# Kernel tuning notes

Hardware: AMD Instinct MI355X
Metric: run time of the kernel (lower is better)

Reference implementation:

```python
import jax, jax.numpy as jnp
import numpy as np

V = 50257; CTX = 2048; D = 1024; H = 16; L = 8; DH = D // H
B = 2; S = 2048; EPS = 1e-5


def setup_inputs() -> dict:
    key = jax.random.key(0)
    ks = jax.random.split(key, 8)
    s = 0.02
    def n(k, shape):
        return jax.random.normal(k, shape, jnp.float32) * s
    return {
        "x": jax.random.randint(ks[0], (B, S), 0, V),
        "wte": n(ks[1], (V, D)),
        "wpe": n(ks[2], (CTX, D)),
        "ln1_g": jnp.ones((L, D), jnp.float32), "ln1_b": jnp.zeros((L, D), jnp.float32),
        "w_qkv": n(ks[3], (L, D, 3 * D)), "b_qkv": jnp.zeros((L, 3 * D), jnp.float32),
        "w_proj": n(ks[4], (L, D, D)), "b_proj": jnp.zeros((L, D), jnp.float32),
        "ln2_g": jnp.ones((L, D), jnp.float32), "ln2_b": jnp.zeros((L, D), jnp.float32),
        "w_fc": n(ks[5], (L, D, 4 * D)), "b_fc": jnp.zeros((L, 4 * D), jnp.float32),
        "w_cp": n(ks[6], (L, 4 * D, D)), "b_cp": jnp.zeros((L, D), jnp.float32),
        "lnf_g": jnp.ones((D,), jnp.float32), "lnf_b": jnp.zeros((D,), jnp.float32),
        "w_head": n(ks[7], (D, V)),
    }


def layernorm(x, g, b):
    m = x.mean(-1, keepdims=True)
    v = ((x - m) ** 2).mean(-1, keepdims=True)
    return (x - m) * jax.lax.rsqrt(v + EPS) * g + b


def gpt_forward(x, wte, wpe, ln1_g, ln1_b, w_qkv, b_qkv, w_proj, b_proj,
                ln2_g, ln2_b, w_fc, b_fc, w_cp, b_cp, lnf_g, lnf_b, w_head):
    Bx, Sx = x.shape
    h = wte[x] + wpe[:Sx]                       # [B,S,D]
    mask = jnp.tril(jnp.ones((Sx, Sx), bool))   # causal mask
    scale = DH ** -0.5

    def block(h, p):
        g1, b1, wq, bq, wp, bp, g2, b2, wf, bf, wc, bc = p
        y = layernorm(h, g1, b1)
        qkv = y @ wq + bq                        # [B,S,3D]
        q, k, v = jnp.split(qkv, 3, axis=-1)
        q = q.reshape(Bx, Sx, H, DH)
        k = k.reshape(Bx, Sx, H, DH)
        v = v.reshape(Bx, Sx, H, DH)
        att = jnp.einsum('bqhd,bkhd->bhqk', q, k) * scale
        att = jnp.where(mask, att, -jnp.inf)
        att = jax.nn.softmax(att, axis=-1)
        z = jnp.einsum('bhqk,bkhd->bqhd', att, v).reshape(Bx, Sx, D)
        h = h + z @ wp + bp
        y2 = layernorm(h, g2, b2)
        h = h + jax.nn.gelu(y2 @ wf + bf, approximate=False) @ wc + bc
        return h, None

    h, _ = jax.lax.scan(block, h, (ln1_g, ln1_b, w_qkv, b_qkv, w_proj, b_proj,
                                   ln2_g, ln2_b, w_fc, b_fc, w_cp, b_cp))
    h = layernorm(h, lnf_g, lnf_b)
    logits = h[:, -1:, :] @ w_head              # [B,1,V] (last position only)
    return logits


def reference(x, wte, wpe, ln1_g, ln1_b, w_qkv, b_qkv, w_proj, b_proj,
              ln2_g, ln2_b, w_fc, b_fc, w_cp, b_cp, lnf_g, lnf_b, w_head):
    return gpt_forward(x, wte, wpe, ln1_g, ln1_b, w_qkv, b_qkv, w_proj, b_proj,
                       ln2_g, ln2_b, w_fc, b_fc, w_cp, b_cp, lnf_g, lnf_b, w_head)
```

## Files before the change

kernel.cpp:

```cpp
#include <hip/hip_runtime.h>
#include <hip/hip_bf16.h>
#include <math.h>

#define VOCAB 50257
#define CTX 2048
#define DMODEL 1024
#define NHEAD 16
#define NLAYER 8
#define DHEAD 64
#define BATCH 2
#define SEQ 2048
#define NTOK (BATCH * SEQ)

typedef __bf16 bf16x8 __attribute__((ext_vector_type(8)));
typedef float  f32x4  __attribute__((ext_vector_type(4)));
typedef unsigned short ushort4v __attribute__((ext_vector_type(4)));
typedef unsigned short ushort8v __attribute__((ext_vector_type(8)));

__device__ inline void gl_lds16(const void* g, void* l) {
    __builtin_amdgcn_global_load_lds(
        (const __attribute__((address_space(1))) unsigned int*)g,
        (__attribute__((address_space(3))) unsigned int*)l, 16, 0, 0);
}

__device__ inline unsigned short f2bs(float v) {
    __hip_bfloat16 t = __float2bfloat16(v);
    return *(unsigned short*)&t;
}

__global__ void embed_kernel(const int* __restrict__ x,
                             const float* __restrict__ wte,
                             const float* __restrict__ wpe,
                             float* __restrict__ h) {
    int t = blockIdx.x;
    int s = t & (SEQ - 1);
    int tok = x[t];
    const float* pe = wpe + (long)s * DMODEL;
    const float* te = wte + (long)tok * DMODEL;
    float* ph = h + (long)t * DMODEL;
    for (int d = threadIdx.x; d < DMODEL; d += 256)
        ph[d] = te[d] + pe[d];
}

__device__ inline float wave_sum(float v) {
    for (int off = 32; off; off >>= 1) v += __shfl_xor(v, off);
    return v;
}
__device__ inline void st_val(float* p, float v) { *p = v; }
__device__ inline void st_val(__hip_bfloat16* p, float v) { *p = __float2bfloat16(v); }

template<typename OT>
__global__ void ln_kernel(const float* __restrict__ in, OT* __restrict__ out,
                          const float* __restrict__ g, const float* __restrict__ b,
                          long row_stride) {
    int row = blockIdx.x;
    const float* px = in + (long)row * row_stride;
    OT* po = out + (long)row * DMODEL;
    int tid = threadIdx.x;
    int wid = tid >> 6, lane = tid & 63;

    float x[4];
    float s = 0.f;
    #pragma unroll
    for (int i = 0; i < 4; ++i) { x[i] = px[tid + i * 256]; s += x[i]; }
    s = wave_sum(s);
    __shared__ float red[4], red2[4];
    if (lane == 0) red[wid] = s;
    __syncthreads();
    float mean = (red[0] + red[1] + red[2] + red[3]) * (1.0f / DMODEL);

    float s2 = 0.f;
    #pragma unroll
    for (int i = 0; i < 4; ++i) { float d = x[i] - mean; s2 += d * d; }
    s2 = wave_sum(s2);
    if (lane == 0) red2[wid] = s2;
    __syncthreads();
    float var = (red2[0] + red2[1] + red2[2] + red2[3]) * (1.0f / DMODEL);
    float r = 1.0f / sqrtf(var + 1e-5f);
    #pragma unroll
    for (int i = 0; i < 4; ++i) {
        int d = tid + i * 256;
        st_val(po + d, (x[i] - mean) * r * g[d] + b[d]);
    }
}

__global__ void convT64(const float* __restrict__ W,
                        unsigned short* __restrict__ WT, int K, int N) {
    __shared__ float t[64][65];
    const int k0 = blockIdx.x * 64, n0 = blockIdx.y * 64;
    const int tid = threadIdx.x;
    {
        const int krow = tid >> 4, c4 = (tid & 15) * 4;
        #pragma unroll
        for (int p = 0; p < 4; ++p) {
            f32x4 gv = *(const f32x4*)&W[(long)(k0 + p * 16 + krow) * N + n0 + c4];
            #pragma unroll
            for (int j = 0; j < 4; ++j) t[p * 16 + krow][c4 + j] = gv[j];
        }
    }
    __syncthreads();
    {
        const int n = tid >> 3, kl = (tid & 7) * 8;
        #pragma unroll
        for (int p = 0; p < 2; ++p) {
            ushort8v pk;
            #pragma unroll
            for (int j = 0; j < 8; ++j) pk[j] = f2bs(t[kl + j][p * 32 + n]);
            *(ushort8v*)&WT[(long)(n0 + p * 32 + n) * K + k0 + kl] = pk;
        }
    }
}

template<int EPI>
__global__ __launch_bounds__(256)
void mm_mfma(const unsigned short* __restrict__ A,
             const unsigned short* __restrict__ BT,
             const float* __restrict__ bias, const float* __restrict__ R,
             void* __restrict__ Cout, int M, int N, int K) {
    __shared__ unsigned short As[128 * 32];
    __shared__ unsigned short Bs[128 * 32];
    const int tid = threadIdx.x;
    const int w = tid >> 6, lane = tid & 63;
    const int bm = blockIdx.y * 128, bn = blockIdx.x * 128;
    const int wr = (w >> 1) * 64, wc = (w & 1) * 64;

    f32x4 acc[4][4];
    #pragma unroll
    for (int m = 0; m < 4; ++m)
        #pragma unroll
        for (int n = 0; n < 4; ++n)
            acc[m][n] = (f32x4){0.f, 0.f, 0.f, 0.f};

    const int lrow = lane >> 2;
    const int lcol = (lane & 3) * 8;
    const unsigned short* gA = A + (long)(bm + w * 32 + lrow) * K + lcol;
    const unsigned short* gB = BT + (long)(bn + w * 32 + lrow) * K + lcol;
    unsigned short* lA = &As[(w * 32) * 32];
    unsigned short* lB = &Bs[(w * 32) * 32];

    for (int k0 = 0; k0 < K; k0 += 32) {
        gl_lds16(gA + k0,          lA);
        gl_lds16(gA + k0 + 16 * K, lA + 16 * 32);
        gl_lds16(gB + k0,          lB);
        gl_lds16(gB + k0 + 16 * K, lB + 16 * 32);
        __syncthreads();

        bf16x8 a[4], b[4];
        #pragma unroll
        for (int m = 0; m < 4; ++m)
            a[m] = *(const bf16x8*)&As[(wr + m * 16 + (lane & 15)) * 32 + (lane >> 4) * 8];
        #pragma unroll
        for (int n = 0; n < 4; ++n)
            b[n] = *(const bf16x8*)&Bs[(wc + n * 16 + (lane & 15)) * 32 + (lane >> 4) * 8];
        #pragma unroll
        for (int m = 0; m < 4; ++m)
            #pragma unroll
            for (int n = 0; n < 4; ++n)
                acc[m][n] = __builtin_amdgcn_mfma_f32_16x16x32_bf16(a[m], b[n], acc[m][n], 0, 0, 0);
        __syncthreads();
    }

    const int r0 = (lane >> 4) * 4, cc = lane & 15;
    #pragma unroll
    for (int n = 0; n < 4; ++n) {
        int colb = bn + wc + n * 16;
        float bv = bias[colb + cc];
        #pragma unroll
        for (int m = 0; m < 4; ++m) {
            int rowb = bm + wr + m * 16 + r0;
            if (EPI == 3) {
                unsigned short* qkvB = (unsigned short*)Cout;
                int which = colb >> 10, hh = (colb & 1023) >> 6, dbase = colb & 63;
                int b_ = rowb >> 11, s_ = rowb & 2047;
                long bh2 = b_ * 16 + hh;
                float v[4];
                #pragma unroll
                for (int r = 0; r < 4; ++r) v[r] = acc[m][n][r] + bv;
                if (which == 2) {
                    ushort4v pk;
                    #pragma unroll
                    for (int r = 0; r < 4; ++r) pk[r] = f2bs(v[r]);
                    *(ushort4v*)&qkvB[8388608L + (bh2 * 64 + dbase + cc) * 2048 + s_] = pk;
                } else {
                    unsigned short* dst = qkvB + (long)which * 4194304L +
                                          (bh2 * 2048 + s_) * 64 + dbase + cc;
                    #pragma unroll
                    for (int r = 0; r < 4; ++r) dst[r * 64] = f2bs(v[r]);
                }
            } else {
                #pragma unroll
                for (int r = 0; r < 4; ++r) {
                    long row = rowb + r, col = colb + cc;
                    float v = acc[m][n][r] + bv;
                    v = 0.5f * v * (1.0f + erff(v * 0.70710678118f));
                    ((__hip_bfloat16*)Cout)[row * N + col] = __float2bfloat16(v);
                }
            }
        }
    }
}

__global__ __launch_bounds__(256)
void mm_mfma_n64(const unsigned short* __restrict__ A,
                 const unsigned short* __restrict__ BT,
                 const float* __restrict__ bias, const float* __restrict__ R,
                 float* __restrict__ Cout, int M, int N, int K) {
    __shared__ unsigned short As[128 * 32];
    __shared__ unsigned short Bs[64 * 32];
    const int tid = threadIdx.x;
    const int w = tid >> 6, lane = tid & 63;
    const int bm = blockIdx.y * 128, bn = blockIdx.x * 64;
    const int wr = (w >> 1) * 64, wc = (w & 1) * 32;

    f32x4 acc[4][2];
    #pragma unroll
    for (int m = 0; m < 4; ++m)
        #pragma unroll
        for (int n = 0; n < 2; ++n)
            acc[m][n] = (f32x4){0.f, 0.f, 0.f, 0.f};

    const int lrow = lane >> 2;
    const int lcol = (lane & 3) * 8;
    const unsigned short* gA = A + (long)(bm + w * 32 + lrow) * K + lcol;
    const unsigned short* gB = BT + (long)(bn + w * 16 + lrow) * K + lcol;
    unsigned short* lA = &As[(w * 32) * 32];
    unsigned short* lB = &Bs[(w * 16) * 32];

    for (int k0 = 0; k0 < K; k0 += 32) {
        gl_lds16(gA + k0,          lA);
        gl_lds16(gA + k0 + 16 * K, lA + 16 * 32);
        gl_lds16(gB + k0,          lB);
        __syncthreads();

        bf16x8 a[4], b[2];
        #pragma unroll
        for (int m = 0; m < 4; ++m)
            a[m] = *(const bf16x8*)&As[(wr + m * 16 + (lane & 15)) * 32 + (lane >> 4) * 8];
        #pragma unroll
        for (int n = 0; n < 2; ++n)
            b[n] = *(const bf16x8*)&Bs[(wc + n * 16 + (lane & 15)) * 32 + (lane >> 4) * 8];
        #pragma unroll
        for (int m = 0; m < 4; ++m)
            #pragma unroll
            for (int n = 0; n < 2; ++n)
                acc[m][n] = __builtin_amdgcn_mfma_f32_16x16x32_bf16(a[m], b[n], acc[m][n], 0, 0, 0);
        __syncthreads();
    }

    const int r0 = (lane >> 4) * 4, cc = lane & 15;
    #pragma unroll
    for (int n = 0; n < 2; ++n) {
        int colb = bn + wc + n * 16;
        float bv = bias[colb + cc];
        #pragma unroll
        for (int m = 0; m < 4; ++m) {
            int rowb = bm + wr + m * 16 + r0;
            #pragma unroll
            for (int r = 0; r < 4; ++r) {
                long row = rowb + r, col = colb + cc;
                float v = acc[m][n][r] + bv + R[row * N + col];
                Cout[row * N + col] = v;
            }
        }
    }
}

__global__ __launch_bounds__(256)
void attn_mfma(const unsigned short* __restrict__ qB,
               const unsigned short* __restrict__ kB,
               const unsigned short* __restrict__ vT,
               __hip_bfloat16* __restrict__ z) {
    const int bh = blockIdx.x;
    const int qb = blockIdx.y * 64;
    const int tid = threadIdx.x, w = tid >> 6, lane = tid & 63;
    const int arow = lane & 15, kg = lane >> 4;
    __shared__ unsigned short Ks[128 * 64];
    __shared__ unsigned short Vs[64 * 128];
    __shared__ unsigned short Ps[4][16 * 128];

    const long kvbase = (long)bh * (2048 * 64);

    bf16x8 qa[2];
    {
        const unsigned short* q0 = qB + kvbase + (long)(qb + w * 16 + arow) * 64 + kg * 8;
        qa[0] = *(const bf16x8*)(q0);
        qa[1] = *(const bf16x8*)(q0 + 32);
    }

    f32x4 po[4];
    float mrow[4], lrow[4];
    #pragma unroll
    for (int i = 0; i < 4; ++i) {
        po[i] = (f32x4){0.f, 0.f, 0.f, 0.f};
        mrow[i] = -1e30f; lrow[i] = 0.f;
    }

    const int ksrow = lane >> 3;
    const int kschunk = (lane & 7) ^ ksrow;
    const int vsr = lane >> 4;
    const int cmax = qb >> 7;

    for (int c = 0; c <= cmax; ++c) {
        {
            const unsigned short* ks0 = kB + kvbase +
                (long)(c * 128 + w * 32 + ksrow) * 64 + kschunk * 8;
            #pragma unroll
            for (int i = 0; i < 4; ++i)
                gl_lds16(ks0 + (long)i * 8 * 64, &Ks[(w * 32 + i * 8) * 64]);
            #pragma unroll
            for (int i = 0; i < 4; ++i) {
                int d = w * 16 + i * 4 + vsr;
                int sch = (lane & 15) ^ (d & 7);
                gl_lds16(vT + kvbase + (long)d * 2048 + c * 128 + sch * 8,
                         &Vs[(w * 16 + i * 4) * 128]);
            }
        }
        __syncthreads();

        f32x4 s[8];
        #pragma unroll
        for (int n = 0; n < 8; ++n) {
            s[n] = (f32x4){0.f, 0.f, 0.f, 0.f};
            int row = n * 16 + arow, sw = row & 7;
            bf16x8 kb0 = *(const bf16x8*)&Ks[row * 64 + (kg ^ sw) * 8];
            bf16x8 kb1 = *(const bf16x8*)&Ks[row * 64 + ((4 + kg) ^ sw) * 8];
            s[n] = __builtin_amdgcn_mfma_f32_16x16x32_bf16(qa[0], kb0, s[n], 0, 0, 0);
            s[n] = __builtin_amdgcn_mfma_f32_16x16x32_bf16(qa[1], kb1, s[n], 0, 0, 0);
        }

        const bool diag = (c == cmax);
        #pragma unroll
        for (int n = 0; n < 8; ++n)
            #pragma unroll
            for (int r = 0; r < 4; ++r) {
                float v = s[n][r] * 0.125f;
                if (diag) {
                    int key = c * 128 + n * 16 + arow;
                    int qrow = qb + w * 16 + kg * 4 + r;
                    if (key > qrow) v = -1e30f;
                }
                s[n][r] = v;
            }

        #pragma unroll
        for (int r = 0; r < 4; ++r) {
            float rm = s[0][r];
            #pragma unroll
            for (int n = 1; n < 8; ++n) rm = fmaxf(rm, s[n][r]);
            #pragma unroll
            for (int off = 1; off < 16; off <<= 1)
                rm = fmaxf(rm, __shfl_xor(rm, off));
            float mnew = fmaxf(mrow[r], rm);
            float esc = expf(mrow[r] - mnew);
            float rs = 0.f;
            #pragma unroll
            for (int n = 0; n < 8; ++n) {
                float p = expf(s[n][r] - mnew);
                s[n][r] = p;
                rs += p;
            }
            #pragma unroll
            for (int off = 1; off < 16; off <<= 1)
                rs += __shfl_xor(rs, off);
            lrow[r] = lrow[r] * esc + rs;
            #pragma unroll
            for (int dt = 0; dt < 4; ++dt) po[dt][r] *= esc;
            mrow[r] = mnew;
        }

        #pragma unroll
        for (int n = 0; n < 8; ++n) {
            int col = n * 16 + arow;
            int chunk = col >> 3, cw = col & 7;
            #pragma unroll
            for (int r = 0; r < 4; ++r) {
                int row = kg * 4 + r;
                Ps[w][row * 128 + ((chunk ^ (row & 7)) * 8 + cw)] = f2bs(s[n][r]);
            }
        }

        bf16x8 pa[4];
        #pragma unroll
        for (int ks = 0; ks < 4; ++ks)
            pa[ks] = *(const bf16x8*)&Ps[w][arow * 128 + (((ks * 4 + kg) ^ (arow & 7)) * 8)];
        #pragma unroll
        for (int dt = 0; dt < 4; ++dt) {
            int vrow = dt * 16 + arow, sw = vrow & 7;
            #pragma unroll
            for (int ks = 0; ks < 4; ++ks) {
                bf16x8 vb = *(const bf16x8*)&Vs[vrow * 128 + (((ks * 4 + kg) ^ sw) * 8)];
                po[dt] = __builtin_amdgcn_mfma_f32_16x16x32_bf16(pa[ks], vb, po[dt], 0, 0, 0);
            }
        }
        __syncthreads();
    }

    const int b_ = bh >> 4, hofs = (bh & 15) * 64;
    #pragma unroll
    for (int dt = 0; dt < 4; ++dt)
        #pragma unroll
        for (int r = 0; r < 4; ++r) {
            long row = (long)b_ * 2048 + qb + w * 16 + kg * 4 + r;
            z[row * 1024 + hofs + dt * 16 + arow] = __float2bfloat16(po[dt][r] / lrow[r]);
        }
}

__global__ void head_kernel(const float* __restrict__ hl, const float* __restrict__ W,
                            float* __restrict__ out) {
    __shared__ float hs[2 * DMODEL];
    int tid = threadIdx.x;
    #pragma unroll
    for (int i = 0; i < 8; ++i) hs[tid + i * 256] = hl[tid + i * 256];
    __syncthreads();
    int v = blockIdx.x * 256 + tid;
    if (v >= VOCAB) return;
    float a0 = 0.f, a1 = 0.f;
    for (int d = 0; d < DMODEL; ++d) {
        float wv = W[(long)d * VOCAB + v];
        a0 += hs[d] * wv;
        a1 += hs[DMODEL + d] * wv;
    }
    out[v] = a0;
    out[VOCAB + v] = a1;
}

extern "C" void kernel_launch(void* const* d_in, const int* in_sizes, int n_in,
                              void* d_out, int out_size, void* d_ws, size_t ws_size,
                              hipStream_t stream) {
    const int*   x      = (const int*)  d_in[0];
    const float* wte    = (const float*)d_in[1];
    const float* wpe    = (const float*)d_in[2];
    const float* ln1_g  = (const float*)d_in[3];
    const float* ln1_b  = (const float*)d_in[4];
    const float* w_qkv  = (const float*)d_in[5];
    const float* b_qkv  = (const float*)d_in[6];
    const float* w_proj = (const float*)d_in[7];
    const float* b_proj = (const float*)d_in[8];
    const float* ln2_g  = (const float*)d_in[9];
    const float* ln2_b  = (const float*)d_in[10];
    const float* w_fc   = (const float*)d_in[11];
    const float* b_fc   = (const float*)d_in[12];
    const float* w_cp   = (const float*)d_in[13];
    const float* b_cp   = (const float*)d_in[14];
    const float* lnf_g  = (const float*)d_in[15];
    const float* lnf_b  = (const float*)d_in[16];
    const float* w_head = (const float*)d_in[17];
    float* out = (float*)d_out;

    char* ws = (char*)d_ws;
    float*          h     = (float*)ws;
    unsigned short* qkvB  = (unsigned short*)(ws + (16L << 20));
    __hip_bfloat16* y_bf  = (__hip_bfloat16*)(ws + (40L << 20));
    __hip_bfloat16* z_bf  = (__hip_bfloat16*)(ws + (48L << 20));
    __hip_bfloat16* fc_bf = (__hip_bfloat16*)(ws + (56L << 20));
    unsigned short* wT    = (unsigned short*)(ws + (88L << 20));
    float*          hl    = (float*)(ws + (97L << 20));

    embed_kernel<<<NTOK, 256, 0, stream>>>(x, wte, wpe, h);

    for (int l = 0; l < NLAYER; ++l) {
        ln_kernel<__hip_bfloat16><<<NTOK, 256, 0, stream>>>(
            h, y_bf, ln1_g + l * DMODEL, ln1_b + l * DMODEL, DMODEL);

        convT64<<<dim3(1024 / 64, 3072 / 64), 256, 0, stream>>>(
            w_qkv + (long)l * DMODEL * 3072, wT, 1024, 3072);
        mm_mfma<3><<<dim3(24, 32), 256, 0, stream>>>(
            (const unsigned short*)y_bf, wT, b_qkv + l * 3072, nullptr, qkvB,
            NTOK, 3072, 1024);

        attn_mfma<<<dim3(BATCH * NHEAD, SEQ / 64), 256, 0, stream>>>(
            qkvB, qkvB + 4194304L, qkvB + 8388608L, z_bf);

        convT64<<<dim3(1024 / 64, 1024 / 64), 256, 0, stream>>>(
            w_proj + (long)l * DMODEL * DMODEL, wT, 1024, 1024);
        mm_mfma_n64<<<dim3(16, 32), 256, 0, stream>>>(
            (const unsigned short*)z_bf, wT, b_proj + l * DMODEL, h, h,
            NTOK, 1024, 1024);

        ln_kernel<__hip_bfloat16><<<NTOK, 256, 0, stream>>>(
            h, y_bf, ln2_g + l * DMODEL, ln2_b + l * DMODEL, DMODEL);

        convT64<<<dim3(1024 / 64, 4096 / 64), 256, 0, stream>>>(
            w_fc + (long)l * DMODEL * 4096, wT, 1024, 4096);
        mm_mfma<2><<<dim3(32, 32), 256, 0, stream>>>(
            (const unsigned short*)y_bf, wT, b_fc + l * 4096, nullptr, fc_bf,
            NTOK, 4096, 1024);

        convT64<<<dim3(4096 / 64, 1024 / 64), 256, 0, stream>>>(
            w_cp + (long)l * 4096 * DMODEL, wT, 4096, 1024);
        mm_mfma_n64<<<dim3(16, 32), 256, 0, stream>>>(
            (const unsigned short*)fc_bf, wT, b_cp + l * DMODEL, h, h,
            NTOK, 1024, 4096);
    }

    ln_kernel<float><<<BATCH, 256, 0, stream>>>(h + (long)(SEQ - 1) * DMODEL, hl,
                                                lnf_g, lnf_b, (long)SEQ * DMODEL);
    head_kernel<<<(VOCAB + 255) / 256, 256, 0, stream>>>(hl, w_head, out);
}
```

Baseline: 2.727 ms.

## Co-schedule weight transpose kernels with LN, attention and FC via block-range fusion

Each weight conversion/transposition is folded into a neighbouring independent kernel (layernorm, attention, FC GEMM) through a block-index split, with two alternating wT buffers so the next weight can be prepared while the current one is consumed. This cuts kernel launches and lets the small, memory-bound transpose work overlap compute-bound work instead of running serially. Using dynamic shared memory sized for the larger branch can lower occupancy for the lighter branch, and mixed-block kernels may cause load imbalance.

```diff
diff --git a/kernel.cpp b/kernel.cpp
--- a/kernel.cpp
+++ b/kernel.cpp
@@ -46,16 +46,14 @@
     for (int off = 32; off; off >>= 1) v += __shfl_xor(v, off);
     return v;
 }
-__device__ inline void st_val(float* p, float v) { *p = v; }
-__device__ inline void st_val(__hip_bfloat16* p, float v) { *p = __float2bfloat16(v); }
-
-template<typename OT>
-__global__ void ln_kernel(const float* __restrict__ in, OT* __restrict__ out,
-                          const float* __restrict__ g, const float* __restrict__ b,
-                          long row_stride) {
-    int row = blockIdx.x;
-    const float* px = in + (long)row * row_stride;
-    OT* po = out + (long)row * DMODEL;
+
+__device__ void ln_body(char* smem, int row, const float* __restrict__ in,
+                        unsigned short* __restrict__ out,
+                        const float* __restrict__ g, const float* __restrict__ b) {
+    float* red  = (float*)smem;
+    float* red2 = red + 4;
+    const float* px = in + (long)row * DMODEL;
+    unsigned short* po = out + (long)row * DMODEL;
     int tid = threadIdx.x;
     int wid = tid >> 6, lane = tid & 63;
 
@@ -64,7 +62,6 @@
     #pragma unroll
     for (int i = 0; i < 4; ++i) { x[i] = px[tid + i * 256]; s += x[i]; }
     s = wave_sum(s);
-    __shared__ float red[4], red2[4];
     if (lane == 0) red[wid] = s;
     __syncthreads();
     float mean = (red[0] + red[1] + red[2] + red[3]) * (1.0f / DMODEL);
@@ -80,14 +77,46 @@
     #pragma unroll
     for (int i = 0; i < 4; ++i) {
         int d = tid + i * 256;
-        st_val(po + d, (x[i] - mean) * r * g[d] + b[d]);
-    }
-}
-
-__global__ void convT64(const float* __restrict__ W,
-                        unsigned short* __restrict__ WT, int K, int N) {
-    __shared__ float t[64][65];
-    const int k0 = blockIdx.x * 64, n0 = blockIdx.y * 64;
+        po[d] = f2bs((x[i] - mean) * r * g[d] + b[d]);
+    }
+}
+
+__global__ void ln_final(const float* __restrict__ in, float* __restrict__ out,
+                         const float* __restrict__ g, const float* __restrict__ b,
+                         long row_stride) {
+    __shared__ float red[4], red2[4];
+    int row = blockIdx.x;
+    const float* px = in + (long)row * row_stride;
+    float* po = out + (long)row * DMODEL;
+    int tid = threadIdx.x;
+    int wid = tid >> 6, lane = tid & 63;
+    float x[4];
+    float s = 0.f;
+    #pragma unroll
+    for (int i = 0; i < 4; ++i) { x[i] = px[tid + i * 256]; s += x[i]; }
+    s = wave_sum(s);
+    if (lane == 0) red[wid] = s;
+    __syncthreads();
+    float mean = (red[0] + red[1] + red[2] + red[3]) * (1.0f / DMODEL);
+    float s2 = 0.f;
+    #pragma unroll
+    for (int i = 0; i < 4; ++i) { float d = x[i] - mean; s2 += d * d; }
+    s2 = wave_sum(s2);
+    if (lane == 0) red2[wid] = s2;
+    __syncthreads();
+    float var = (red2[0] + red2[1] + red2[2] + red2[3]) * (1.0f / DMODEL);
+    float r = 1.0f / sqrtf(var + 1e-5f);
+    #pragma unroll
+    for (int i = 0; i < 4; ++i) {
+        int d = tid + i * 256;
+        po[d] = (x[i] - mean) * r * g[d] + b[d];
+    }
+}
+
+__device__ void convT_body(char* smem, int kx, int ny, const float* __restrict__ W,
+                           unsigned short* __restrict__ WT, int K, int N) {
+    float (*t)[65] = (float(*)[65])smem;
+    const int k0 = kx * 64, n0 = ny * 64;
     const int tid = threadIdx.x;
     {
         const int krow = tid >> 4, c4 = (tid & 15) * 4;
@@ -111,12 +140,11 @@
     }
 }
 
-template<int EPI>
 __global__ __launch_bounds__(256)
-void mm_mfma(const unsigned short* __restrict__ A,
-             const unsigned short* __restrict__ BT,
-             const float* __restrict__ bias, const float* __restrict__ R,
-             void* __restrict__ Cout, int M, int N, int K) {
+void mm_qkv(const unsigned short* __restrict__ A,
+            const unsigned short* __restrict__ BT,
+            const float* __restrict__ bias,
+            unsigned short* __restrict__ qkvB, int M, int N, int K) {
     __shared__ unsigned short As[128 * 32];
     __shared__ unsigned short Bs[128 * 32];
     const int tid = threadIdx.x;
@@ -168,33 +196,89 @@
         #pragma unroll
         for (int m = 0; m < 4; ++m) {
             int rowb = bm + wr + m * 16 + r0;
-            if (EPI == 3) {
-                unsigned short* qkvB = (unsigned short*)Cout;
-                int which = colb >> 10, hh = (colb & 1023) >> 6, dbase = colb & 63;
-                int b_ = rowb >> 11, s_ = rowb & 2047;
-                long bh2 = b_ * 16 + hh;
-                float v[4];
+            int which = colb >> 10, hh = (colb & 1023) >> 6, dbase = colb & 63;
+            int b_ = rowb >> 11, s_ = rowb & 2047;
+            long bh2 = b_ * 16 + hh;
+            float v[4];
+            #pragma unroll
+            for (int r = 0; r < 4; ++r) v[r] = acc[m][n][r] + bv;
+            if (which == 2) {
+                ushort4v pk;
                 #pragma unroll
-                for (int r = 0; r < 4; ++r) v[r] = acc[m][n][r] + bv;
-                if (which == 2) {
-                    ushort4v pk;
-                    #pragma unroll
-                    for (int r = 0; r < 4; ++r) pk[r] = f2bs(v[r]);
-                    *(ushort4v*)&qkvB[8388608L + (bh2 * 64 + dbase + cc) * 2048 + s_] = pk;
-                } else {
-                    unsigned short* dst = qkvB + (long)which * 4194304L +
-                                          (bh2 * 2048 + s_) * 64 + dbase + cc;
-                    #pragma unroll
-                    for (int r = 0; r < 4; ++r) dst[r * 64] = f2bs(v[r]);
-                }
+                for (int r = 0; r < 4; ++r) pk[r] = f2bs(v[r]);
+                *(ushort4v*)&qkvB[8388608L + (bh2 * 64 + dbase + cc) * 2048 + s_] = pk;
             } else {
+                unsigned short* dst = qkvB + (long)which * 4194304L +
+                                      (bh2 * 2048 + s_) * 64 + dbase + cc;
                 #pragma unroll
-                for (int r = 0; r < 4; ++r) {
-                    long row = rowb + r, col = colb + cc;
-                    float v = acc[m][n][r] + bv;
-                    v = 0.5f * v * (1.0f + erff(v * 0.70710678118f));
-                    ((__hip_bfloat16*)Cout)[row * N + col] = __float2bfloat16(v);
-                }
+                for (int r = 0; r < 4; ++r) dst[r * 64] = f2bs(v[r]);
+            }
+        }
+    }
+}
+
+__device__ void mm128_gelu_body(char* smem, int bx, int by,
+                                const unsigned short* __restrict__ A,
+                                const unsigned short* __restrict__ BT,
+                                const float* __restrict__ bias,
+                                unsigned short* __restrict__ Cout, int M, int N, int K) {
+    unsigned short* As = (unsigned short*)smem;
+    unsigned short* Bs = As + 128 * 32;
+    const int tid = threadIdx.x;
+    const int w = tid >> 6, lane = tid & 63;
+    const int bm = by * 128, bn = bx * 128;
+    const int wr = (w >> 1) * 64, wc = (w & 1) * 64;
+
+    f32x4 acc[4][4];
+    #pragma unroll
+    for (int m = 0; m < 4; ++m)
+        #pragma unroll
+        for (int n = 0; n < 4; ++n)
+            acc[m][n] = (f32x4){0.f, 0.f, 0.f, 0.f};
+
+    const int lrow = lane >> 2;
+    const int lcol = (lane & 3) * 8;
+    const unsigned short* gA = A + (long)(bm + w * 32 + lrow) * K + lcol;
+    const unsigned short* gB = BT + (long)(bn + w * 32 + lrow) * K + lcol;
+    unsigned short* lA = &As[(w * 32) * 32];
+    unsigned short* lB = &Bs[(w * 32) * 32];
+
+    for (int k0 = 0; k0 < K; k0 += 32) {
+        gl_lds16(gA + k0,          lA);
+        gl_lds16(gA + k0 + 16 * K, lA + 16 * 32);
+        gl_lds16(gB + k0,          lB);
+        gl_lds16(gB + k0 + 16 * K, lB + 16 * 32);
+        __syncthreads();
+
+        bf16x8 a[4], b[4];
+        #pragma unroll
+        for (int m = 0; m < 4; ++m)
+            a[m] = *(const bf16x8*)&As[(wr + m * 16 + (lane & 15)) * 32 + (lane >> 4) * 8];
+        #pragma unroll
+        for (int n = 0; n < 4; ++n)
+            b[n] = *(const bf16x8*)&Bs[(wc + n * 16 + (lane & 15)) * 32 + (lane >> 4) * 8];
+        #pragma unroll
+        for (int m = 0; m < 4; ++m)
+            #pragma unroll
+            for (int n = 0; n < 4; ++n)
+                acc[m][n] = __builtin_amdgcn_mfma_f32_16x16x32_bf16(a[m], b[n], acc[m][n], 0, 0, 0);
+        __syncthreads();
+    }
+
+    const int r0 = (lane >> 4) * 4, cc = lane & 15;
+    #pragma unroll
+    for (int n = 0; n < 4; ++n) {
+        int colb = bn + wc + n * 16;
+        float bv = bias[colb + cc];
+        #pragma unroll
+        for (int m = 0; m < 4; ++m) {
+            int rowb = bm + wr + m * 16 + r0;
+            #pragma unroll
+            for (int r = 0; r < 4; ++r) {
+                long row = rowb + r, col = colb + cc;
+                float v = acc[m][n][r] + bv;
+                v = 0.5f * v * (1.0f + erff(v * 0.70710678118f));
+                Cout[row * N + col] = f2bs(v);
             }
         }
     }
@@ -265,18 +349,16 @@
     }
 }
 
-__global__ __launch_bounds__(256)
-void attn_mfma(const unsigned short* __restrict__ qB,
-               const unsigned short* __restrict__ kB,
-               const unsigned short* __restrict__ vT,
-               __hip_bfloat16* __restrict__ z) {
-    const int bh = blockIdx.x;
-    const int qb = blockIdx.y * 64;
+__device__ void attn_body(char* smem, int bh, int qb,
+                          const unsigned short* __restrict__ qB,
+                          const unsigned short* __restrict__ kB,
+                          const unsigned short* __restrict__ vT,
+                          __hip_bfloat16* __restrict__ z) {
     const int tid = threadIdx.x, w = tid >> 6, lane = tid & 63;
     const int arow = lane & 15, kg = lane >> 4;
-    __shared__ unsigned short Ks[128 * 64];
-    __shared__ unsigned short Vs[64 * 128];
-    __shared__ unsigned short Ps[4][16 * 128];
+    unsigned short* Ks = (unsigned short*)smem;
+    unsigned short* Vs = Ks + 128 * 64;
+    unsigned short* Ps = Vs + 64 * 128 + w * 16 * 128;
 
     const long kvbase = (long)bh * (2048 * 64);
 
@@ -375,14 +457,14 @@
             #pragma unroll
             for (int r = 0; r < 4; ++r) {
                 int row = kg * 4 + r;
-                Ps[w][row * 128 + ((chunk ^ (row & 7)) * 8 + cw)] = f2bs(s[n][r]);
+                Ps[row * 128 + ((chunk ^ (row & 7)) * 8 + cw)] = f2bs(s[n][r]);
             }
         }
 
         bf16x8 pa[4];
         #pragma unroll
         for (int ks = 0; ks < 4; ++ks)
-            pa[ks] = *(const bf16x8*)&Ps[w][arow * 128 + (((ks * 4 + kg) ^ (arow & 7)) * 8)];
+            pa[ks] = *(const bf16x8*)&Ps[arow * 128 + (((ks * 4 + kg) ^ (arow & 7)) * 8)];
         #pragma unroll
         for (int dt = 0; dt < 4; ++dt) {
             int vrow = dt * 16 + arow, sw = vrow & 7;
@@ -403,6 +485,55 @@
             long row = (long)b_ * 2048 + qb + w * 16 + kg * 4 + r;
             z[row * 1024 + hofs + dt * 16 + arow] = __float2bfloat16(po[dt][r] / lrow[r]);
         }
+}
+
+__global__ __launch_bounds__(256)
+void fused_ln_convT(const float* __restrict__ h, unsigned short* __restrict__ y,
+                    const float* __restrict__ g, const float* __restrict__ b,
+                    const float* __restrict__ W, unsigned short* __restrict__ WT,
+                    int K, int N, int nLN) {
+    extern __shared__ char smem[];
+    int bid = blockIdx.x;
+    if (bid < nLN) {
+        ln_body(smem, bid, h, y, g, b);
+    } else {
+        int r = bid - nLN, kt = K >> 6;
+        convT_body(smem, r % kt, r / kt, W, WT, K, N);
+    }
+}
+
+__global__ __launch_bounds__(256)
+void fused_attn_convT(const unsigned short* __restrict__ qB,
+                      const unsigned short* __restrict__ kB,
+                      const unsigned short* __restrict__ vT,
+                      __hip_bfloat16* __restrict__ z,
+                      const float* __restrict__ W, unsigned short* __restrict__ WT,
+                      int K, int N, int nAttn) {
+    extern __shared__ char smem[];
+    int bid = blockIdx.x;
+    if (bid < nAttn) {
+        attn_body(smem, bid & 31, (bid >> 5) * 64, qB, kB, vT, z);
+    } else {
+        int r = bid - nAttn, kt = K >> 6;
+        convT_body(smem, r % kt, r / kt, W, WT, K, N);
+    }
+}
+
+__global__ __launch_bounds__(256)
+void fused_fc_convT(const unsigned short* __restrict__ A,
+                    const unsigned short* __restrict__ BT,
+                    const float* __restrict__ bias, unsigned short* __restrict__ Cout,
+                    int M, int N, int K,
+                    const float* __restrict__ W2, unsigned short* __restrict__ WT2,
+                    int K2, int N2, int nMM) {
+    extern __shared__ char smem[];
+    int bid = blockIdx.x;
+    if (bid < nMM) {
+        mm128_gelu_body(smem, bid & 31, bid >> 5, A, BT, bias, Cout, M, N, K);
+    } else {
+        int r = bid - nMM, kt = K2 >> 6;
+        convT_body(smem, r % kt, r / kt, W2, WT2, K2, N2);
+    }
 }
 
 __global__ void head_kernel(const float* __restrict__ hl, const float* __restrict__ W,
@@ -450,50 +581,47 @@
     char* ws = (char*)d_ws;
     float*          h     = (float*)ws;
     unsigned short* qkvB  = (unsigned short*)(ws + (16L << 20));
-    __hip_bfloat16* y_bf  = (__hip_bfloat16*)(ws + (40L << 20));
+    unsigned short* y_bf  = (unsigned short*)(ws + (40L << 20));
     __hip_bfloat16* z_bf  = (__hip_bfloat16*)(ws + (48L << 20));
-    __hip_bfloat16* fc_bf = (__hip_bfloat16*)(ws + (56L << 20));
-    unsigned short* wT    = (unsigned short*)(ws + (88L << 20));
-    float*          hl    = (float*)(ws + (97L << 20));
+    unsigned short* fc_bf = (unsigned short*)(ws + (56L << 20));
+    unsigned short* wT_a  = (unsigned short*)(ws + (88L << 20));
+    unsigned short* wT_b  = (unsigned short*)(ws + (97L << 20));
+    float*          hl    = (float*)(ws + (106L << 20));
+
+    const int SM_CONV = 16640;
+    const int SM_ATTN = 49152;
 
     embed_kernel<<<NTOK, 256, 0, stream>>>(x, wte, wpe, h);
 
     for (int l = 0; l < NLAYER; ++l) {
-        ln_kernel<__hip_bfloat16><<<NTOK, 256, 0, stream>>>(
-            h, y_bf, ln1_g + l * DMODEL, ln1_b + l * DMODEL, DMODEL);
-
-        convT64<<<dim3(1024 / 64, 3072 / 64), 256, 0, stream>>>(
-            w_qkv + (long)l * DMODEL * 3072, wT, 1024, 3072);
-        mm_mfma<3><<<dim3(24, 32), 256, 0, stream>>>(
-            (const unsigned short*)y_bf, wT, b_qkv + l * 3072, nullptr, qkvB,
-            NTOK, 3072, 1024);
-
-        attn_mfma<<<dim3(BATCH * NHEAD, SEQ / 64), 256, 0, stream>>>(
-            qkvB, qkvB + 4194304L, qkvB + 8388608L, z_bf);
-
-        convT64<<<dim3(1024 / 64, 1024 / 64), 256, 0, stream>>>(
-            w_proj + (long)l * DMODEL * DMODEL, wT, 1024, 1024);
+        fused_ln_convT<<<4096 + 768, 256, SM_CONV, stream>>>(
+            h, y_bf, ln1_g + l * DMODEL, ln1_b + l * DMODEL,
+            w_qkv + (long)l * DMODEL * 3072, wT_a, 1024, 3072, 4096);
+
+        mm_qkv<<<dim3(24, 32), 256, 0, stream>>>(
+            y_bf, wT_a, b_qkv + l * 3072, qkvB, NTOK, 3072, 1024);
+
+        fused_attn_convT<<<1024 + 256, 256, SM_ATTN, stream>>>(
+            qkvB, qkvB + 4194304L, qkvB + 8388608L, z_bf,
+            w_proj + (long)l * DMODEL * DMODEL, wT_b, 1024, 1024, 1024);
+
         mm_mfma_n64<<<dim3(16, 32), 256, 0, stream>>>(
-            (const unsigned short*)z_bf, wT, b_proj + l * DMODEL, h, h,
+            (const unsigned short*)z_bf, wT_b, b_proj + l * DMODEL, h, h,
             NTOK, 1024, 1024);
 
-        ln_kernel<__hip_bfloat16><<<NTOK, 256, 0, stream>>>(
-            h, y_bf, ln2_g + l * DMODEL, ln2_b + l * DMODEL, DMODEL);
-
-        convT64<<<dim3(1024 / 64, 4096 / 64), 256, 0, stream>>>(
-            w_fc + (long)l * DMODEL * 4096, wT, 1024, 4096);
-        mm_mfma<2><<<dim3(32, 32), 256, 0, stream>>>(
-            (const unsigned short*)y_bf, wT, b_fc + l * 4096, nullptr, fc_bf,
-            NTOK, 4096, 1024);
-
-        convT64<<<dim3(4096 / 64, 1024 / 64), 256, 0, stream>>>(
-            w_cp + (long)l * 4096 * DMODEL, wT, 4096, 1024);
+        fused_ln_convT<<<4096 + 1024, 256, SM_CONV, stream>>>(
+            h, y_bf, ln2_g + l * DMODEL, ln2_b + l * DMODEL,
+            w_fc + (long)l * DMODEL * 4096, wT_a, 1024, 4096, 4096);
+
+        fused_fc_convT<<<1024 + 1024, 256, SM_CONV, stream>>>(
+            y_bf, wT_a, b_fc + l * 4096, fc_bf, NTOK, 4096, 1024,
+            w_cp + (long)l * 4096 * DMODEL, wT_b, 4096, 1024, 1024);
+
         mm_mfma_n64<<<dim3(16, 32), 256, 0, stream>>>(
-            (const unsigned short*)fc_bf, wT, b_cp + l * DMODEL, h, h,
-            NTOK, 1024, 4096);
-    }
-
-    ln_kernel<float><<<BATCH, 256, 0, stream>>>(h + (long)(SEQ - 1) * DMODEL, hl,
-                                                lnf_g, lnf_b, (long)SEQ * DMODEL);
+            fc_bf, wT_b, b_cp + l * DMODEL, h, h, NTOK, 1024, 4096);
+    }
+
+    ln_final<<<BATCH, 256, 0, stream>>>(h + (long)(SEQ - 1) * DMODEL, hl,
+                                        lnf_g, lnf_b, (long)SEQ * DMODEL);
     head_kernel<<<(VOCAB + 255) / 256, 256, 0, stream>>>(hl, w_head, out);
 }
```

Result: faster. 2.667 ms (-2.2%).
